# Optimization experiments

Hardware: AMD Instinct MI355X
Metric: run time of the kernel (lower is better)

Reference implementation:

```python
import jax, jax.numpy as jnp
import numpy as np


def setup_inputs() -> dict:
    key = jax.random.key(0)
    B, C, H, W, A, G = 16, 512, 16, 16, 64, 256
    # Ragged group sizes (constant, deterministic) -> padded gather indices + mask
    rng = np.random.default_rng(0)
    sizes = rng.integers(32, 257, size=G)
    N = int(sizes.sum())          # ~36849 total sound tokens
    S_max = int(sizes.max())      # 256
    offsets = np.concatenate([[0], np.cumsum(sizes)[:-1]])
    pad_idx = np.zeros((G, S_max), dtype=np.int64)
    pad_mask = np.zeros((G, S_max), dtype=bool)
    for g in range(G):
        s = int(sizes[g])
        pad_idx[g, :s] = offsets[g] + np.arange(s)
        pad_mask[g, :s] = True
    k1, k2 = jax.random.split(key)
    return {
        'Z_img': jax.random.normal(k1, (B, C, H, W), jnp.float32),
        'Z_snd': jax.random.normal(k2, (N, C), jnp.float32),
        'pad_idx': jnp.asarray(pad_idx),
        'pad_mask': jnp.asarray(pad_mask),
        'attn_dims': A,
    }


def reference(Z_img, Z_snd, pad_idx, pad_mask, attn_dims):
    # Eval-mode forward of AudioAttention (no random subsampling).
    C = Z_img.shape[1]
    A = attn_dims
    # Global-average-pool image features: [B, C, H, W] -> [B, C]
    z = Z_img.reshape(Z_img.shape[0], C, -1).mean(axis=2)
    z_img, query = z[:, : C - A], z[:, C - A :]          # [B, C-A], [B, A]
    # Ragged groups as padded gather: [G, S, C]
    snd = Z_snd[pad_idx]
    value, key_ = snd[..., : C - A], snd[..., C - A :]   # [G,S,C-A], [G,S,A]
    # Per-group cross attention with the shared image queries
    scores = jnp.einsum('ba,gsa->gbs', query, key_)      # [G, B, S]
    scores = jnp.where(pad_mask[:, None, :], scores, -jnp.inf)
    attn = jax.nn.softmax(scores, axis=-1)               # padded cols -> 0 weight
    M_snd = jnp.einsum('gbs,gsc->gbc', attn, value)      # [G, B, C-A]
    M_img = jnp.broadcast_to(z_img[None], M_snd.shape)   # [G, B, C-A]
    return M_img, M_snd
```

## Files before the change

### kernel.cpp

```cpp
#include <hip/hip_runtime.h>
#include <math.h>

#define B_  16
#define C_  512
#define A_  64
#define CV  448
#define G_  256
#define HW  256
#define SMX 256
#define BSP 8

__global__ __launch_bounds__(256) void meanpool_kernel(const float* __restrict__ Zimg,
                                                       float* __restrict__ z) {
  int row  = (blockIdx.x << 2) + (threadIdx.x >> 6);
  int lane = threadIdx.x & 63;
  const float4* p = (const float4*)(Zimg + (size_t)row * HW);
  float4 v = p[lane];
  float s = (v.x + v.y) + (v.z + v.w);
  #pragma unroll
  for (int off = 32; off > 0; off >>= 1)
    s += __shfl_down(s, off, 64);
  if (lane == 0) z[row] = s * (1.0f / HW);
}

__global__ __launch_bounds__(256) void score_kernel(
    const float* __restrict__ Zsnd,
    const int*   __restrict__ pad_idx,
    const float* __restrict__ z,
    float*       __restrict__ attnW,
    int Smax, int N)
{
  const int bid  = blockIdx.x;
  const int g    = bid >> 1;
  const int b0   = (bid & 1) * BSP;
  const int t    = threadIdx.x;
  const int lane = t & 63;
  const int wave = t >> 6;

  __shared__ float qs[BSP * A_];
  __shared__ float red[4 * BSP];
  __shared__ float red2[4 * BSP];

  int myidx = -1;
  if (t < Smax) {
    int v = pad_idx[(size_t)g * Smax + t];
    bool ok = ((t == 0) || (v != 0)) && (v >= 0) && (v < N);
    myidx = ok ? v : -1;
  }
  const bool valid = (myidx >= 0);

  if (t < BSP * 16) {
    int b = t >> 4, a4 = t & 15;
    *(float4*)(qs + b * A_ + a4 * 4) =
        *(const float4*)(z + (b0 + b) * C_ + CV + a4 * 4);
  }
  __syncthreads();

  const float* krow = Zsnd + (size_t)(valid ? myidx : 0) * C_ + CV;
  float4 kv[16];
  #pragma unroll
  for (int a4 = 0; a4 < 16; a4++)
    kv[a4] = *(const float4*)(krow + a4 * 4);

  float sc[BSP];
  #pragma unroll
  for (int b = 0; b < BSP; b++) sc[b] = 0.0f;

  #pragma unroll 2
  for (int a4 = 0; a4 < 16; a4++) {
    #pragma unroll
    for (int b = 0; b < BSP; b++) {
      float4 qv = *(const float4*)(qs + b * A_ + a4 * 4);
      sc[b] += qv.x * kv[a4].x + qv.y * kv[a4].y +
               qv.z * kv[a4].z + qv.w * kv[a4].w;
    }
  }

  #pragma unroll
  for (int b = 0; b < BSP; b++) {
    float v = valid ? sc[b] : -INFINITY;
    #pragma unroll
    for (int off = 32; off > 0; off >>= 1)
      v = fmaxf(v, __shfl_xor(v, off, 64));
    if (lane == 0) red[wave * BSP + b] = v;
  }
  __syncthreads();

  float ex[BSP];
  #pragma unroll
  for (int b = 0; b < BSP; b++) {
    float gm = fmaxf(fmaxf(red[0 * BSP + b], red[1 * BSP + b]),
                     fmaxf(red[2 * BSP + b], red[3 * BSP + b]));
    float e = valid ? __expf(sc[b] - gm) : 0.0f;
    ex[b] = e;
    float es = e;
    #pragma unroll
    for (int off = 32; off > 0; off >>= 1)
      es += __shfl_xor(es, off, 64);
    if (lane == 0) red2[wave * BSP + b] = es;
  }
  __syncthreads();

  #pragma unroll
  for (int b = 0; b < BSP; b++) {
    float gs = (red2[0 * BSP + b] + red2[1 * BSP + b]) +
               (red2[2 * BSP + b] + red2[3 * BSP + b]);
    attnW[((size_t)g * B_ + b0 + b) * SMX + t] = ex[b] / gs;
  }
}

__global__ __launch_bounds__(256) void out_kernel(
    const float* __restrict__ Zsnd,
    const int*   __restrict__ pad_idx,
    const float* __restrict__ attnW,
    const float* __restrict__ z,
    float*       __restrict__ Mimg,
    float*       __restrict__ Msnd,
    int Smax, int N)
{
  const int bid  = blockIdx.x;
  const int g    = bid >> 2;
  const int cs   = bid & 3;
  const int c0   = cs * 128;
  const int w    = (cs == 3) ? 64 : 128;
  const int t    = threadIdx.x;
  const int lane = t & 63;
  const int wave = t >> 6;
  const int cl   = lane & 31;
  const int h    = lane >> 5;

  __shared__ int   idxs[SMX];
  __shared__ float attnS[B_ * SMX];
  __shared__ int   redi[4];

  int myidx = 0, sgv = 0;
  if (t < Smax) {
    int v = pad_idx[(size_t)g * Smax + t];
    bool ok = ((t == 0) || (v != 0)) && (v >= 0) && (v < N);
    myidx = ok ? v : 0;
    sgv   = ok ? (t + 1) : 0;
  }
  idxs[t] = myidx;
  #pragma unroll
  for (int off = 32; off > 0; off >>= 1)
    sgv = max(sgv, __shfl_xor(sgv, off, 64));
  if (lane == 0) redi[wave] = sgv;

  #pragma unroll
  for (int i = 0; i < 4; i++) {
    int li = i * 256 + t;
    *(float4*)(attnS + li * 4) = *(const float4*)(attnW + (size_t)g * (B_ * SMX) + li * 4);
  }

  if (w == 128) {
    #pragma unroll
    for (int i = 0; i < 2; i++) {
      int li = i * 256 + t;
      int b = li >> 5, c4 = li & 31;
      *(float4*)(Mimg + (size_t)g * (B_ * CV) + b * CV + c0 + c4 * 4) =
          *(const float4*)(z + b * C_ + c0 + c4 * 4);
    }
  } else {
    int b = t >> 4, c4 = t & 15;
    *(float4*)(Mimg + (size_t)g * (B_ * CV) + b * CV + c0 + c4 * 4) =
        *(const float4*)(z + b * C_ + c0 + c4 * 4);
  }

  __syncthreads();
  const int sg   = max(max(redi[0], redi[1]), max(redi[2], redi[3]));
  const int sg16 = (sg + 15) & ~15;

  const int b0 = wave * 4;
  const float* vbase = Zsnd + c0 + cl * 4;
  float4 a0 = make_float4(0.f, 0.f, 0.f, 0.f);
  float4 a1 = make_float4(0.f, 0.f, 0.f, 0.f);
  float4 a2 = make_float4(0.f, 0.f, 0.f, 0.f);
  float4 a3 = make_float4(0.f, 0.f, 0.f, 0.f);

  for (int s0 = 0; s0 < sg16; s0 += 16) {
    float4 v[8];
    #pragma unroll
    for (int j = 0; j < 8; j++) {
      int idx = idxs[s0 + 2 * j + h];
      v[j] = *(const float4*)(vbase + (size_t)idx * C_);
    }
    #pragma unroll
    for (int j = 0; j < 8; j++) {
      int so = s0 + 2 * j + h;
      float w0 = attnS[(b0 + 0) * SMX + so];
      float w1 = attnS[(b0 + 1) * SMX + so];
      float w2 = attnS[(b0 + 2) * SMX + so];
      float w3 = attnS[(b0 + 3) * SMX + so];
      float4 vv = v[j];
      a0.x += w0 * vv.x; a0.y += w0 * vv.y; a0.z += w0 * vv.z; a0.w += w0 * vv.w;
      a1.x += w1 * vv.x; a1.y += w1 * vv.y; a1.z += w1 * vv.z; a1.w += w1 * vv.w;
      a2.x += w2 * vv.x; a2.y += w2 * vv.y; a2.z += w2 * vv.z; a2.w += w2 * vv.w;
      a3.x += w3 * vv.x; a3.y += w3 * vv.y; a3.z += w3 * vv.z; a3.w += w3 * vv.w;
    }
  }

  a0.x += __shfl_xor(a0.x, 32, 64); a0.y += __shfl_xor(a0.y, 32, 64);
  a0.z += __shfl_xor(a0.z, 32, 64); a0.w += __shfl_xor(a0.w, 32, 64);
  a1.x += __shfl_xor(a1.x, 32, 64); a1.y += __shfl_xor(a1.y, 32, 64);
  a1.z += __shfl_xor(a1.z, 32, 64); a1.w += __shfl_xor(a1.w, 32, 64);
  a2.x += __shfl_xor(a2.x, 32, 64); a2.y += __shfl_xor(a2.y, 32, 64);
  a2.z += __shfl_xor(a2.z, 32, 64); a2.w += __shfl_xor(a2.w, 32, 64);
  a3.x += __shfl_xor(a3.x, 32, 64); a3.y += __shfl_xor(a3.y, 32, 64);
  a3.z += __shfl_xor(a3.z, 32, 64); a3.w += __shfl_xor(a3.w, 32, 64);

  if (h == 0 && cl * 4 < w) {
    float* obase = Msnd + (size_t)g * (B_ * CV) + (size_t)b0 * CV + c0 + cl * 4;
    *(float4*)(obase + 0 * CV) = a0;
    *(float4*)(obase + 1 * CV) = a1;
    *(float4*)(obase + 2 * CV) = a2;
    *(float4*)(obase + 3 * CV) = a3;
  }
}

extern "C" void kernel_launch(void* const* d_in, const int* in_sizes, int n_in,
                              void* d_out, int out_size, void* d_ws, size_t ws_size,
                              hipStream_t stream) {
  const float* Zimg   = (const float*)d_in[0];
  const float* Zsnd   = (const float*)d_in[1];
  const int*   padidx = (const int*)d_in[2];

  const int N    = in_sizes[1] / C_;
  const int Smax = in_sizes[2] / G_;

  float* z     = (float*)d_ws;
  float* attnW = z + B_ * C_;
  float* Mimg  = (float*)d_out;
  float* Msnd  = Mimg + (size_t)G_ * B_ * CV;

  meanpool_kernel<<<(B_ * C_) / 4, 256, 0, stream>>>(Zimg, z);
  score_kernel<<<G_ * 2, 256, 0, stream>>>(Zsnd, padidx, z, attnW, Smax, N);
  out_kernel<<<G_ * 4, 256, 0, stream>>>(Zsnd, padidx, attnW, z, Mimg, Msnd, Smax, N);
}
```

Measured before the change: 176.3 us.

## Transpose attention weights to [S,B] and split out_kernel waves across batch and tokens

```diff
diff --git a/kernel.cpp b/kernel.cpp
--- a/kernel.cpp
+++ b/kernel.cpp
@@ -57,23 +57,29 @@
   __syncthreads();
 
   const float* krow = Zsnd + (size_t)(valid ? myidx : 0) * C_ + CV;
-  float4 kv[16];
-  #pragma unroll
-  for (int a4 = 0; a4 < 16; a4++)
-    kv[a4] = *(const float4*)(krow + a4 * 4);
-
   float sc[BSP];
   #pragma unroll
   for (int b = 0; b < BSP; b++) sc[b] = 0.0f;
 
-  #pragma unroll 2
-  for (int a4 = 0; a4 < 16; a4++) {
+  #pragma unroll
+  for (int c = 0; c < 4; c++) {
+    float4 k0 = *(const float4*)(krow + c * 16 + 0);
+    float4 k1 = *(const float4*)(krow + c * 16 + 4);
+    float4 k2 = *(const float4*)(krow + c * 16 + 8);
+    float4 k3 = *(const float4*)(krow + c * 16 + 12);
     #pragma unroll
     for (int b = 0; b < BSP; b++) {
-      float4 qv = *(const float4*)(qs + b * A_ + a4 * 4);
-      sc[b] += qv.x * kv[a4].x + qv.y * kv[a4].y +
-               qv.z * kv[a4].z + qv.w * kv[a4].w;
-    }
+      const float* qb = qs + b * A_ + c * 16;
+      float4 q0 = *(const float4*)(qb + 0);
+      float4 q1 = *(const float4*)(qb + 4);
+      float4 q2 = *(const float4*)(qb + 8);
+      float4 q3 = *(const float4*)(qb + 12);
+      sc[b] += q0.x * k0.x + q0.y * k0.y + q0.z * k0.z + q0.w * k0.w
+             + q1.x * k1.x + q1.y * k1.y + q1.z * k1.z + q1.w * k1.w
+             + q2.x * k2.x + q2.y * k2.y + q2.z * k2.z + q2.w * k2.w
+             + q3.x * k3.x + q3.y * k3.y + q3.z * k3.z + q3.w * k3.w;
+    }
+    __builtin_amdgcn_sched_barrier(0);
   }
 
   #pragma unroll
@@ -101,12 +107,21 @@
   }
   __syncthreads();
 
-  #pragma unroll
-  for (int b = 0; b < BSP; b++) {
-    float gs = (red2[0 * BSP + b] + red2[1 * BSP + b]) +
-               (red2[2 * BSP + b] + red2[3 * BSP + b]);
-    attnW[((size_t)g * B_ + b0 + b) * SMX + t] = ex[b] / gs;
-  }
+  float* orow = attnW + ((size_t)g * SMX + t) * B_ + b0;
+  float4 o0, o1;
+  {
+    float iv[BSP];
+    #pragma unroll
+    for (int b = 0; b < BSP; b++) {
+      float gs = (red2[0 * BSP + b] + red2[1 * BSP + b]) +
+                 (red2[2 * BSP + b] + red2[3 * BSP + b]);
+      iv[b] = ex[b] / gs;
+    }
+    o0 = make_float4(iv[0], iv[1], iv[2], iv[3]);
+    o1 = make_float4(iv[4], iv[5], iv[6], iv[7]);
+  }
+  *(float4*)(orow + 0) = o0;
+  *(float4*)(orow + 4) = o1;
 }
 
 __global__ __launch_bounds__(256) void out_kernel(
@@ -128,9 +143,12 @@
   const int wave = t >> 6;
   const int cl   = lane & 31;
   const int h    = lane >> 5;
-
+  const int bh   = wave & 1;
+  const int sh   = wave >> 1;
+  const int b0   = bh * 8;
+
+  __shared__ float attnT[SMX * B_];
   __shared__ int   idxs[SMX];
-  __shared__ float attnS[B_ * SMX];
   __shared__ int   redi[4];
 
   int myidx = 0, sgv = 0;
@@ -149,7 +167,7 @@
   #pragma unroll
   for (int i = 0; i < 4; i++) {
     int li = i * 256 + t;
-    *(float4*)(attnS + li * 4) = *(const float4*)(attnW + (size_t)g * (B_ * SMX) + li * 4);
+    *(float4*)(attnT + li * 4) = *(const float4*)(attnW + (size_t)g * (SMX * B_) + li * 4);
   }
 
   if (w == 128) {
@@ -170,50 +188,60 @@
   const int sg   = max(max(redi[0], redi[1]), max(redi[2], redi[3]));
   const int sg16 = (sg + 15) & ~15;
 
-  const int b0 = wave * 4;
   const float* vbase = Zsnd + c0 + cl * 4;
-  float4 a0 = make_float4(0.f, 0.f, 0.f, 0.f);
-  float4 a1 = make_float4(0.f, 0.f, 0.f, 0.f);
-  float4 a2 = make_float4(0.f, 0.f, 0.f, 0.f);
-  float4 a3 = make_float4(0.f, 0.f, 0.f, 0.f);
+  float4 acc[8];
+  #pragma unroll
+  for (int b = 0; b < 8; b++) acc[b] = make_float4(0.f, 0.f, 0.f, 0.f);
 
   for (int s0 = 0; s0 < sg16; s0 += 16) {
-    float4 v[8];
-    #pragma unroll
-    for (int j = 0; j < 8; j++) {
-      int idx = idxs[s0 + 2 * j + h];
+    float4 v[4];
+    int so[4];
+    #pragma unroll
+    for (int j = 0; j < 4; j++) {
+      so[j] = s0 + 4 * j + 2 * sh + h;
+      int idx = idxs[so[j]];
       v[j] = *(const float4*)(vbase + (size_t)idx * C_);
     }
     #pragma unroll
-    for (int j = 0; j < 8; j++) {
-      int so = s0 + 2 * j + h;
-      float w0 = attnS[(b0 + 0) * SMX + so];
-      float w1 = attnS[(b0 + 1) * SMX + so];
-      float w2 = attnS[(b0 + 2) * SMX + so];
-      float w3 = attnS[(b0 + 3) * SMX + so];
+    for (int j = 0; j < 4; j++) {
+      float4 w0 = *(const float4*)(attnT + so[j] * B_ + b0);
+      float4 w1 = *(const float4*)(attnT + so[j] * B_ + b0 + 4);
       float4 vv = v[j];
-      a0.x += w0 * vv.x; a0.y += w0 * vv.y; a0.z += w0 * vv.z; a0.w += w0 * vv.w;
-      a1.x += w1 * vv.x; a1.y += w1 * vv.y; a1.z += w1 * vv.z; a1.w += w1 * vv.w;
-      a2.x += w2 * vv.x; a2.y += w2 * vv.y; a2.z += w2 * vv.z; a2.w += w2 * vv.w;
-      a3.x += w3 * vv.x; a3.y += w3 * vv.y; a3.z += w3 * vv.z; a3.w += w3 * vv.w;
-    }
-  }
-
-  a0.x += __shfl_xor(a0.x, 32, 64); a0.y += __shfl_xor(a0.y, 32, 64);
-  a0.z += __shfl_xor(a0.z, 32, 64); a0.w += __shfl_xor(a0.w, 32, 64);
-  a1.x += __shfl_xor(a1.x, 32, 64); a1.y += __shfl_xor(a1.y, 32, 64);
-  a1.z += __shfl_xor(a1.z, 32, 64); a1.w += __shfl_xor(a1.w, 32, 64);
-  a2.x += __shfl_xor(a2.x, 32, 64); a2.y += __shfl_xor(a2.y, 32, 64);
-  a2.z += __shfl_xor(a2.z, 32, 64); a2.w += __shfl_xor(a2.w, 32, 64);
-  a3.x += __shfl_xor(a3.x, 32, 64); a3.y += __shfl_xor(a3.y, 32, 64);
-  a3.z += __shfl_xor(a3.z, 32, 64); a3.w += __shfl_xor(a3.w, 32, 64);
-
-  if (h == 0 && cl * 4 < w) {
-    float* obase = Msnd + (size_t)g * (B_ * CV) + (size_t)b0 * CV + c0 + cl * 4;
-    *(float4*)(obase + 0 * CV) = a0;
-    *(float4*)(obase + 1 * CV) = a1;
-    *(float4*)(obase + 2 * CV) = a2;
-    *(float4*)(obase + 3 * CV) = a3;
+      acc[0].x += w0.x * vv.x; acc[0].y += w0.x * vv.y; acc[0].z += w0.x * vv.z; acc[0].w += w0.x * vv.w;
+      acc[1].x += w0.y * vv.x; acc[1].y += w0.y * vv.y; acc[1].z += w0.y * vv.z; acc[1].w += w0.y * vv.w;
+      acc[2].x += w0.z * vv.x; acc[2].y += w0.z * vv.y; acc[2].z += w0.z * vv.z; acc[2].w += w0.z * vv.w;
+      acc[3].x += w0.w * vv.x; acc[3].y += w0.w * vv.y; acc[3].z += w0.w * vv.z; acc[3].w += w0.w * vv.w;
+      acc[4].x += w1.x * vv.x; acc[4].y += w1.x * vv.y; acc[4].z += w1.x * vv.z; acc[4].w += w1.x * vv.w;
+      acc[5].x += w1.y * vv.x; acc[5].y += w1.y * vv.y; acc[5].z += w1.y * vv.z; acc[5].w += w1.y * vv.w;
+      acc[6].x += w1.z * vv.x; acc[6].y += w1.z * vv.y; acc[6].z += w1.z * vv.z; acc[6].w += w1.z * vv.w;
+      acc[7].x += w1.w * vv.x; acc[7].y += w1.w * vv.y; acc[7].z += w1.w * vv.z; acc[7].w += w1.w * vv.w;
+    }
+  }
+
+  __syncthreads();
+  float* redS = attnT;
+  if (sh == 1) {
+    #pragma unroll
+    for (int b = 0; b < 8; b++)
+      *(float4*)(redS + (((size_t)bh * 8 + b) * 64 + lane) * 4) = acc[b];
+  }
+  __syncthreads();
+  if (sh == 0) {
+    #pragma unroll
+    for (int b = 0; b < 8; b++) {
+      float4 o = *(const float4*)(redS + (((size_t)bh * 8 + b) * 64 + lane) * 4);
+      acc[b].x += o.x; acc[b].y += o.y; acc[b].z += o.z; acc[b].w += o.w;
+      acc[b].x += __shfl_xor(acc[b].x, 32, 64);
+      acc[b].y += __shfl_xor(acc[b].y, 32, 64);
+      acc[b].z += __shfl_xor(acc[b].z, 32, 64);
+      acc[b].w += __shfl_xor(acc[b].w, 32, 64);
+    }
+    if (h == 0 && cl * 4 < w) {
+      float* obase = Msnd + (size_t)g * (B_ * CV) + (size_t)b0 * CV + c0 + cl * 4;
+      #pragma unroll
+      for (int b = 0; b < 8; b++)
+        *(float4*)(obase + b * CV) = acc[b];
+    }
   }
 }
 
```

Result: faster. 160.5 us (-9.0%).
